# Optimization experiments

Hardware: AMD Instinct MI355X
Metric: run time of the kernel (lower is better)

Reference implementation:

```python
import jax, jax.numpy as jnp
import numpy as np
from jax import lax

EMBED_DIM = 512
HIDDEN_DIM = 256
OUT_DIM = HIDDEN_DIM // 2
BATCH = 32
SEQ = 4096
THRESHOLD = 1.0
DECAY = 0.95
REFRACTORY = 2.0


def setup_inputs() -> dict:
    key = jax.random.key(0)
    k1, k2, k3 = jax.random.split(key, 3)
    x = jax.random.normal(k1, (BATCH, SEQ, EMBED_DIM), dtype=jnp.float32)
    input_weights = jax.random.normal(k2, (EMBED_DIM, HIDDEN_DIM), dtype=jnp.float32) * 0.1
    hidden_weights = jax.random.normal(k3, (HIDDEN_DIM, OUT_DIM), dtype=jnp.float32) * 0.1
    return {"x": x, "input_weights": input_weights, "hidden_weights": hidden_weights}


def reference(x, input_weights, hidden_weights):
    B, S, D = x.shape
    H = input_weights.shape[1]
    dt = x.dtype
    # batch-mean then project all timesteps at once: [S, H]
    currents = jnp.einsum('sd,dh->sh', x.mean(0), input_weights)

    def step(carry, ic):
        mem, refr = carry
        active = (refr <= 0).astype(dt)
        mem = DECAY * mem + ic * active
        spikes = (mem >= THRESHOLD).astype(dt)
        mem = mem * (1.0 - spikes)
        refr = jnp.maximum(refr - 1.0, 0.0) + spikes * REFRACTORY
        return (mem, refr), spikes

    init = (jnp.zeros((H,), dt), jnp.zeros((H,), dt))
    _, spikes = lax.scan(step, init, currents)  # spikes: [S, H]
    out = spikes @ hidden_weights               # [S, OUT]
    out_mean = out.mean(0)                      # mean over timesteps
    # original repeats the (batch-independent) output across the batch
    return jnp.broadcast_to(out_mean, (B, out_mean.shape[0]))
```

## Files before the change

### kernel.cpp

```cpp
#include <hip/hip_runtime.h>
#include <stdint.h>


#define S_LEN 4096
#define D_DIM 512
#define H_DIM 256
#define O_DIM 128
#define B_SZ  32
#define TS    8
#define CH    64
#define NCH   (S_LEN / CH)
#define ROWS  (CH / 4)

typedef const __attribute__((address_space(1))) void  glob_void;
typedef       __attribute__((address_space(3))) void  lds_void;

__global__ __launch_bounds__(256)
void fused_mean_proj(const float4* __restrict__ x4,
                     const float*  __restrict__ iw,
                     float4*       __restrict__ cur4,
                     float*        __restrict__ out) {
    __shared__ float4 xm4[TS * D_DIM / 4];
    const int t   = threadIdx.x;
    const int s0  = blockIdx.x * TS;
    const int SD4 = S_LEN * D_DIM / 4;
    const size_t base = (size_t)s0 * (D_DIM / 4);

    if (blockIdx.x == 0) {
        for (int i = t; i < B_SZ * O_DIM; i += 256) out[i] = 0.f;
    }

    float4 acc[4];
    #pragma unroll
    for (int k = 0; k < 4; ++k) acc[k] = make_float4(0.f, 0.f, 0.f, 0.f);

    for (int b = 0; b < B_SZ; b += 2) {
        const float4* p0 = x4 + (size_t)b * SD4 + base;
        const float4* p1 = p0 + SD4;
        float4 v0[4], v1[4];
        #pragma unroll
        for (int k = 0; k < 4; ++k) v0[k] = p0[t + k * 256];
        #pragma unroll
        for (int k = 0; k < 4; ++k) v1[k] = p1[t + k * 256];
        #pragma unroll
        for (int k = 0; k < 4; ++k) {
            acc[k].x += v0[k].x; acc[k].y += v0[k].y; acc[k].z += v0[k].z; acc[k].w += v0[k].w;
            acc[k].x += v1[k].x; acc[k].y += v1[k].y; acc[k].z += v1[k].z; acc[k].w += v1[k].w;
        }
    }
    const float inv = 1.0f / (float)B_SZ;
    #pragma unroll
    for (int k = 0; k < 4; ++k) {
        float4 a = acc[k];
        a.x *= inv; a.y *= inv; a.z *= inv; a.w *= inv;
        xm4[t + k * 256] = a;
    }
    __syncthreads();

    const int h = t;
    float acc2[TS];
    #pragma unroll
    for (int ss = 0; ss < TS; ++ss) acc2[ss] = 0.f;

    for (int d4 = 0; d4 < D_DIM / 4; ++d4) {
        const int d = d4 * 4;
        float w0 = iw[(d + 0) * H_DIM + h];
        float w1 = iw[(d + 1) * H_DIM + h];
        float w2 = iw[(d + 2) * H_DIM + h];
        float w3 = iw[(d + 3) * H_DIM + h];
        #pragma unroll
        for (int ss = 0; ss < TS; ++ss) {
            float4 xv = xm4[ss * (D_DIM / 4) + d4];
            acc2[ss] += xv.x * w0 + xv.y * w1 + xv.z * w2 + xv.w * w3;
        }
    }
    const int g0 = (blockIdx.x * 2) * H_DIM + h;
    cur4[g0]         = make_float4(acc2[0], acc2[1], acc2[2], acc2[3]);
    cur4[g0 + H_DIM] = make_float4(acc2[4], acc2[5], acc2[6], acc2[7]);
}

#define LIF_STEP(IC) {                          \
    float ict = sp2 ? 0.f : (IC);               \
    float tt  = fmaf(0.95f, u, ict);            \
    u   = sp1 ? 0.f : tt;                       \
    bool sp = (u >= 1.0f);                      \
    cnt += sp ? 1 : 0;                          \
    sp2 = sp1; sp1 = sp; }

__global__ __launch_bounds__(64)
void snn_scan_out(const float4* __restrict__ cur4,
                  const float*  __restrict__ hw,
                  float*        __restrict__ out) {
    __shared__ __attribute__((aligned(16))) float4 lbuf[2][ROWS * 64];
    __shared__ float cl[64];
    const int lane  = threadIdx.x;
    const int hbase = blockIdx.x * 64;

    #pragma unroll
    for (int r = 0; r < ROWS; ++r) {
        const float4* g = cur4 + (size_t)r * H_DIM + hbase + lane;
        __builtin_amdgcn_global_load_lds((glob_void*)g,
                                         (lds_void*)&lbuf[0][r * 64 + lane], 16, 0, 0);
    }

    float u = 0.f;
    int   cnt = 0;
    bool  sp1 = false, sp2 = false;

    for (int c = 0; c < NCH; ++c) {
        __syncthreads();
        if (c + 1 < NCH) {
            #pragma unroll
            for (int r = 0; r < ROWS; ++r) {
                const float4* g = cur4 + (size_t)((c + 1) * ROWS + r) * H_DIM + hbase + lane;
                __builtin_amdgcn_global_load_lds((glob_void*)g,
                                                 (lds_void*)&lbuf[(c + 1) & 1][r * 64 + lane],
                                                 16, 0, 0);
            }
        }
        const float4* lb = lbuf[c & 1];
        float4 v[ROWS];
        #pragma unroll
        for (int r = 0; r < ROWS; ++r) v[r] = lb[r * 64 + lane];
        __builtin_amdgcn_sched_barrier(0);

        #pragma unroll
        for (int r = 0; r < ROWS; ++r) {
            LIF_STEP(v[r].x); LIF_STEP(v[r].y); LIF_STEP(v[r].z); LIF_STEP(v[r].w);
        }
    }

    __syncthreads();
    cl[lane] = (float)cnt;
    __syncthreads();
    float a0 = 0.f, a1 = 0.f;
    #pragma unroll 8
    for (int k = 0; k < 64; ++k) {
        float c = cl[k];
        const float* w = hw + (size_t)(hbase + k) * O_DIM;
        a0 = fmaf(c, w[lane], a0);
        a1 = fmaf(c, w[lane + 64], a1);
    }
    a0 *= (1.0f / (float)S_LEN);
    a1 *= (1.0f / (float)S_LEN);
    for (int b = 0; b < B_SZ; ++b) {
        atomicAdd(out + b * O_DIM + lane,      a0);
        atomicAdd(out + b * O_DIM + lane + 64, a1);
    }
}

extern "C" void kernel_launch(void* const* d_in, const int* in_sizes, int n_in,
                              void* d_out, int out_size, void* d_ws, size_t ws_size,
                              hipStream_t stream) {
    const float4* x4 = (const float4*)d_in[0];
    const float*  iw = (const float*) d_in[1];
    const float*  hw = (const float*) d_in[2];
    float* out   = (float*)d_out;
    float4* cur4 = (float4*)d_ws;

    hipLaunchKernelGGL(fused_mean_proj, dim3(S_LEN / TS), dim3(256), 0, stream,
                       x4, iw, cur4, out);
    hipLaunchKernelGGL(snn_scan_out, dim3(4), dim3(64), 0, stream,
                       cur4, hw, out);
}
```

Before: 474.2 us.

## Fuse projection and LIF scan into one producer-consumer kernel with flag sync

Merges the batch-mean/projection kernel and the sequential LIF scan into a single launch. 512 producer blocks write current chunks and bump per-chunk atomic counters, while 4 consumer blocks spin on those flags and start scanning as soon as early chunks are ready. The aim is to overlap the serial scan with the bandwidth-bound projection instead of running them back to back. This depends on the consumer blocks being co-resident with the producers; if they are not, the spin-wait could stall. It also adds two memsets to the launch path.

```diff
diff --git a/kernel.cpp b/kernel.cpp
--- a/kernel.cpp
+++ b/kernel.cpp
@@ -7,77 +7,17 @@
 #define H_DIM 256
 #define O_DIM 128
 #define B_SZ  32
-#define TS    8
+
+#define NPROD 512
+#define NCONS 4
+#define FPB   2
 #define CH    64
 #define NCH   (S_LEN / CH)
 #define ROWS  (CH / 4)
+#define FLAG_GOAL 16u
 
 typedef const __attribute__((address_space(1))) void  glob_void;
 typedef       __attribute__((address_space(3))) void  lds_void;
-
-__global__ __launch_bounds__(256)
-void fused_mean_proj(const float4* __restrict__ x4,
-                     const float*  __restrict__ iw,
-                     float4*       __restrict__ cur4,
-                     float*        __restrict__ out) {
-    __shared__ float4 xm4[TS * D_DIM / 4];
-    const int t   = threadIdx.x;
-    const int s0  = blockIdx.x * TS;
-    const int SD4 = S_LEN * D_DIM / 4;
-    const size_t base = (size_t)s0 * (D_DIM / 4);
-
-    if (blockIdx.x == 0) {
-        for (int i = t; i < B_SZ * O_DIM; i += 256) out[i] = 0.f;
-    }
-
-    float4 acc[4];
-    #pragma unroll
-    for (int k = 0; k < 4; ++k) acc[k] = make_float4(0.f, 0.f, 0.f, 0.f);
-
-    for (int b = 0; b < B_SZ; b += 2) {
-        const float4* p0 = x4 + (size_t)b * SD4 + base;
-        const float4* p1 = p0 + SD4;
-        float4 v0[4], v1[4];
-        #pragma unroll
-        for (int k = 0; k < 4; ++k) v0[k] = p0[t + k * 256];
-        #pragma unroll
-        for (int k = 0; k < 4; ++k) v1[k] = p1[t + k * 256];
-        #pragma unroll
-        for (int k = 0; k < 4; ++k) {
-            acc[k].x += v0[k].x; acc[k].y += v0[k].y; acc[k].z += v0[k].z; acc[k].w += v0[k].w;
-            acc[k].x += v1[k].x; acc[k].y += v1[k].y; acc[k].z += v1[k].z; acc[k].w += v1[k].w;
-        }
-    }
-    const float inv = 1.0f / (float)B_SZ;
-    #pragma unroll
-    for (int k = 0; k < 4; ++k) {
-        float4 a = acc[k];
-        a.x *= inv; a.y *= inv; a.z *= inv; a.w *= inv;
-        xm4[t + k * 256] = a;
-    }
-    __syncthreads();
-
-    const int h = t;
-    float acc2[TS];
-    #pragma unroll
-    for (int ss = 0; ss < TS; ++ss) acc2[ss] = 0.f;
-
-    for (int d4 = 0; d4 < D_DIM / 4; ++d4) {
-        const int d = d4 * 4;
-        float w0 = iw[(d + 0) * H_DIM + h];
-        float w1 = iw[(d + 1) * H_DIM + h];
-        float w2 = iw[(d + 2) * H_DIM + h];
-        float w3 = iw[(d + 3) * H_DIM + h];
-        #pragma unroll
-        for (int ss = 0; ss < TS; ++ss) {
-            float4 xv = xm4[ss * (D_DIM / 4) + d4];
-            acc2[ss] += xv.x * w0 + xv.y * w1 + xv.z * w2 + xv.w * w3;
-        }
-    }
-    const int g0 = (blockIdx.x * 2) * H_DIM + h;
-    cur4[g0]         = make_float4(acc2[0], acc2[1], acc2[2], acc2[3]);
-    cur4[g0 + H_DIM] = make_float4(acc2[4], acc2[5], acc2[6], acc2[7]);
-}
 
 #define LIF_STEP(IC) {                          \
     float ict = sp2 ? 0.f : (IC);               \
@@ -87,36 +27,110 @@
     cnt += sp ? 1 : 0;                          \
     sp2 = sp1; sp1 = sp; }
 
-__global__ __launch_bounds__(64)
-void snn_scan_out(const float4* __restrict__ cur4,
-                  const float*  __restrict__ hw,
-                  float*        __restrict__ out) {
-    __shared__ __attribute__((aligned(16))) float4 lbuf[2][ROWS * 64];
-    __shared__ float cl[64];
-    const int lane  = threadIdx.x;
-    const int hbase = blockIdx.x * 64;
+#define ACC4(A, V) { A.x += V.x; A.y += V.y; A.z += V.z; A.w += V.w; }
 
-    #pragma unroll
-    for (int r = 0; r < ROWS; ++r) {
-        const float4* g = cur4 + (size_t)r * H_DIM + hbase + lane;
-        __builtin_amdgcn_global_load_lds((glob_void*)g,
-                                         (lds_void*)&lbuf[0][r * 64 + lane], 16, 0, 0);
+__global__ __launch_bounds__(256, 2)
+void snn_fused(const float4* __restrict__ x4,
+               const float*  __restrict__ iw,
+               const float*  __restrict__ hw,
+               float4*       __restrict__ cur4,
+               uint32_t*     __restrict__ flags,
+               float*        __restrict__ out) {
+    __shared__ __attribute__((aligned(16))) char smem[2 * ROWS * 64 * 16 + 256];
+    const int t = threadIdx.x;
+
+    if (blockIdx.x < NPROD) {
+        float4* xm = (float4*)smem;
+        const int r2 = t >> 7;
+        const int d4 = t & 127;
+        const int h  = t;
+        const float inv = 1.0f / (float)B_SZ;
+        const size_t bstr = (size_t)S_LEN * (D_DIM / 4);
+
+        for (int g = 0; g < FPB; ++g) {
+            const int f  = blockIdx.x + NPROD * g;
+            const int s0 = 4 * f;
+
+            float4 a0 = make_float4(0.f, 0.f, 0.f, 0.f);
+            float4 a1 = make_float4(0.f, 0.f, 0.f, 0.f);
+            const float4* xb = x4 + (size_t)(s0 + r2) * (D_DIM / 4) + d4;
+            for (int b = 0; b < B_SZ; b += 4) {
+                const float4* p = xb + (size_t)b * bstr;
+                float4 v00 = p[0],            v01 = p[2 * (D_DIM / 4)];
+                float4 v10 = p[bstr],         v11 = p[bstr + 2 * (D_DIM / 4)];
+                float4 v20 = p[2 * bstr],     v21 = p[2 * bstr + 2 * (D_DIM / 4)];
+                float4 v30 = p[3 * bstr],     v31 = p[3 * bstr + 2 * (D_DIM / 4)];
+                ACC4(a0, v00); ACC4(a0, v10); ACC4(a0, v20); ACC4(a0, v30);
+                ACC4(a1, v01); ACC4(a1, v11); ACC4(a1, v21); ACC4(a1, v31);
+            }
+            a0.x *= inv; a0.y *= inv; a0.z *= inv; a0.w *= inv;
+            a1.x *= inv; a1.y *= inv; a1.z *= inv; a1.w *= inv;
+            xm[r2 * (D_DIM / 4) + d4]       = a0;
+            xm[(r2 + 2) * (D_DIM / 4) + d4] = a1;
+            __syncthreads();
+
+            float acc2[4] = {0.f, 0.f, 0.f, 0.f};
+            for (int d4i = 0; d4i < D_DIM / 4; ++d4i) {
+                const int d = d4i * 4;
+                float w0 = iw[(d + 0) * H_DIM + h];
+                float w1 = iw[(d + 1) * H_DIM + h];
+                float w2 = iw[(d + 2) * H_DIM + h];
+                float w3 = iw[(d + 3) * H_DIM + h];
+                #pragma unroll
+                for (int r = 0; r < 4; ++r) {
+                    float4 xv = xm[r * (D_DIM / 4) + d4i];
+                    acc2[r] += xv.x * w0 + xv.y * w1 + xv.z * w2 + xv.w * w3;
+                }
+            }
+            cur4[(size_t)f * H_DIM + h] =
+                make_float4(acc2[0], acc2[1], acc2[2], acc2[3]);
+
+            __syncthreads();
+            if (t == 0) {
+                __builtin_amdgcn_fence(__ATOMIC_RELEASE, "agent");
+                atomicAdd(&flags[f >> 4], 1u);
+            }
+        }
+        return;
     }
+
+    if (t >= 64) return;
+    float4 (*lbuf)[ROWS * 64] = (float4 (*)[ROWS * 64])smem;
+    float* cl = (float*)(smem + 2 * ROWS * 64 * 16);
+    const int lane  = t;
+    const int hbase = (int)(blockIdx.x - NPROD) * 64;
+
+    auto wait_chunk = [&](int c) {
+        if (lane == 0) {
+            while (atomicAdd(&flags[c], 0u) < FLAG_GOAL)
+                __builtin_amdgcn_s_sleep(2);
+        }
+        __builtin_amdgcn_fence(__ATOMIC_ACQUIRE, "agent");
+    };
+    auto stage = [&](int c) {
+        #pragma unroll
+        for (int r = 0; r < ROWS; ++r) {
+            const float4* g = cur4 + (size_t)(c * ROWS + r) * H_DIM + hbase + lane;
+            __builtin_amdgcn_global_load_lds((glob_void*)g,
+                                             (lds_void*)&lbuf[c & 1][r * 64 + lane],
+                                             16, 0, 0);
+        }
+    };
+
+    wait_chunk(0);
+    stage(0);
 
     float u = 0.f;
     int   cnt = 0;
     bool  sp1 = false, sp2 = false;
 
     for (int c = 0; c < NCH; ++c) {
-        __syncthreads();
         if (c + 1 < NCH) {
-            #pragma unroll
-            for (int r = 0; r < ROWS; ++r) {
-                const float4* g = cur4 + (size_t)((c + 1) * ROWS + r) * H_DIM + hbase + lane;
-                __builtin_amdgcn_global_load_lds((glob_void*)g,
-                                                 (lds_void*)&lbuf[(c + 1) & 1][r * 64 + lane],
-                                                 16, 0, 0);
-            }
+            wait_chunk(c + 1);
+            stage(c + 1);
+            asm volatile("s_waitcnt vmcnt(16)" ::: "memory");
+        } else {
+            asm volatile("s_waitcnt vmcnt(0)" ::: "memory");
         }
         const float4* lb = lbuf[c & 1];
         float4 v[ROWS];
@@ -157,9 +171,10 @@
     const float*  hw = (const float*) d_in[2];
     float* out   = (float*)d_out;
     float4* cur4 = (float4*)d_ws;
+    uint32_t* flags = (uint32_t*)((char*)d_ws + (size_t)4 * 1024 * 1024);
 
-    hipLaunchKernelGGL(fused_mean_proj, dim3(S_LEN / TS), dim3(256), 0, stream,
-                       x4, iw, cur4, out);
-    hipLaunchKernelGGL(snn_scan_out, dim3(4), dim3(64), 0, stream,
-                       cur4, hw, out);
+    hipMemsetAsync(flags, 0, NCH * sizeof(uint32_t), stream);
+    hipMemsetAsync(out,   0, B_SZ * O_DIM * sizeof(float), stream);
+    hipLaunchKernelGGL(snn_fused, dim3(NPROD + NCONS), dim3(256), 0, stream,
+                       x4, iw, hw, cur4, flags, out);
 }
```

After: 496.3 us. 1.05x slower.
